# Optimization experiments

Measured on AMD Instinct MI355X. Metric: run time of the kernel, lower is better.

Reference implementation:

```python
import jax, jax.numpy as jnp
import numpy as np

B, S, D, H = 16, 512, 512, 8
DH = D // H
EPS = 1e-5
NEG = -1.0e9


def _layernorm(v, g, b):
    mu = jnp.mean(v, axis=-1, keepdims=True)
    var = jnp.mean(jnp.square(v - mu), axis=-1, keepdims=True)
    return (v - mu) * jax.lax.rsqrt(var + EPS) * g + b


def setup_inputs() -> dict:
    key = jax.random.key(0)
    ks = jax.random.split(key, 12)
    sd = 1.0 / np.sqrt(D)
    return {
        "x": jax.random.normal(ks[0], (B, S, D), dtype=jnp.float32),
        "mask": jax.random.randint(ks[1], (B, S, S), 0, 2, dtype=jnp.int32),
        "ln_g": jnp.ones((D,), jnp.float32),
        "ln_b": jnp.zeros((D,), jnp.float32),
        "lna_g": jnp.ones((S,), jnp.float32),  # LayerNorm over attention scores (last dim = S = model_dim)
        "lna_b": jnp.zeros((S,), jnp.float32),
        "Wq": jax.random.uniform(ks[2], (D, D), jnp.float32, -sd, sd),
        "bq": jnp.zeros((D,), jnp.float32),
        "Wk": jax.random.uniform(ks[3], (D, D), jnp.float32, -sd, sd),
        "bk": jnp.zeros((D,), jnp.float32),
        "Wv": jax.random.uniform(ks[4], (D, D), jnp.float32, -sd, sd),
        "bv": jnp.zeros((D,), jnp.float32),
        "Wd": jax.random.uniform(ks[5], (D, D), jnp.float32, -sd, sd),
        "bd": jnp.zeros((D,), jnp.float32),
    }


def reference(x, mask, ln_g, ln_b, lna_g, lna_b, Wq, bq, Wk, bk, Wv, bv, Wd, bd):
    # pre-LN
    h = _layernorm(x, ln_g, ln_b)  # [B,S,D]
    # projections -> [B,H,S,DH]
    q = (h @ Wq + bq).reshape(B, S, H, DH).transpose(0, 2, 1, 3)
    k = (h @ Wk + bk).reshape(B, S, H, DH).transpose(0, 2, 1, 3)
    v = (h @ Wv + bv).reshape(B, S, H, DH).transpose(0, 2, 1, 3)
    # raw scores [B,H,S,S]
    scores = jnp.einsum("bhqd,bhkd->bhqk", q, k) / jnp.sqrt(jnp.asarray(DH, x.dtype))
    # non-standard: LayerNorm over the key axis of the score matrix
    scores = _layernorm(scores, lna_g, lna_b)
    # mask (broadcast over heads), then softmax
    scores = jnp.where(mask[:, None, :, :] == 0, jnp.asarray(NEG, x.dtype), scores)
    attn = jax.nn.softmax(scores, axis=-1)
    # dropout omitted (eval mode / deterministic reference)
    out = jnp.einsum("bhqk,bhkd->bhqd", attn, v)
    out = out.transpose(0, 2, 1, 3).reshape(B, S, D)
    out = out @ Wd + bd
    return out + x
```

## Files before the change

### kernel.cpp

```cpp
#include <hip/hip_runtime.h>
#include <hip/hip_bf16.h>
#include <stdint.h>


typedef __hip_bfloat16 bf16;
typedef __bf16 bf16x8 __attribute__((ext_vector_type(8)));
typedef float f32x4 __attribute__((ext_vector_type(4)));

#define MFMA16(a, b, c) __builtin_amdgcn_mfma_f32_16x16x32_bf16((a), (b), (c), 0, 0, 0)

static __device__ __forceinline__ bf16 f2b(float v) { return __float2bfloat16(v); }
static __device__ __forceinline__ bf16x8 ld8(const bf16* p) { return *(const bf16x8*)p; }
static __device__ __forceinline__ uint16_t f2bu(float v) {
  return __hip_bfloat16_raw(__float2bfloat16(v)).x;
}
static __device__ __forceinline__ float bu2f(uint32_t u) {
  union { uint32_t i; float f; } c;
  c.i = u << 16;
  return c.f;
}
static __device__ __forceinline__ void stage16(const bf16* g, bf16* l) {
  __builtin_amdgcn_global_load_lds(
      (const __attribute__((address_space(1))) void*)g,
      (__attribute__((address_space(3))) void*)l, 16, 0, 0);
}

__global__ __launch_bounds__(256) void transpose512(
    const float* __restrict__ W0, const float* __restrict__ W1,
    const float* __restrict__ W2, const float* __restrict__ W3,
    bf16* __restrict__ T0, bf16* __restrict__ T1,
    bf16* __restrict__ T2, bf16* __restrict__ T3) {
  __shared__ float t[32][33];
  const float* src; bf16* dst;
  switch (blockIdx.z) {
    case 0: src = W0; dst = T0; break;
    case 1: src = W1; dst = T1; break;
    case 2: src = W2; dst = T2; break;
    default: src = W3; dst = T3; break;
  }
  int tx = threadIdx.x, ty = threadIdx.y;
  int n0 = blockIdx.x * 32, k0 = blockIdx.y * 32;
#pragma unroll
  for (int i = 0; i < 4; i++) {
    int kk = ty * 4 + i;
    t[kk][tx] = src[(k0 + kk) * 512 + n0 + tx];
  }
  __syncthreads();
#pragma unroll
  for (int i = 0; i < 4; i++) {
    int nn = ty * 4 + i;
    dst[(n0 + nn) * 512 + k0 + tx] = f2b(t[tx][nn]);
  }
}

__global__ __launch_bounds__(256) void mask_bits(const int* __restrict__ mask,
                                                 uint32_t* __restrict__ tbits) {
  int t = blockIdx.x * 256 + threadIdx.x;
  int row = t >> 4, l = t & 15;
  const int* mrow = mask + (size_t)row * 512 + l;
  uint32_t o = 0;
#pragma unroll
  for (int j = 0; j < 32; j++) o |= (mrow[j * 16] != 0 ? 1u : 0u) << j;
  tbits[t] = o;
}

__global__ __launch_bounds__(256) void ln_rows(
    const float* __restrict__ x, const float* __restrict__ g,
    const float* __restrict__ be, bf16* __restrict__ h) {
  int row = blockIdx.x;
  int tid = threadIdx.x;
  const float* xr = x + (size_t)row * 512;
  float v0 = xr[tid], v1 = xr[tid + 256];
  float s = v0 + v1, s2 = v0 * v0 + v1 * v1;
#pragma unroll
  for (int m = 1; m < 64; m <<= 1) {
    s += __shfl_xor(s, m);
    s2 += __shfl_xor(s2, m);
  }
  __shared__ float rs[4], rs2[4];
  int w = tid >> 6;
  if ((tid & 63) == 0) { rs[w] = s; rs2[w] = s2; }
  __syncthreads();
  s = rs[0] + rs[1] + rs[2] + rs[3];
  s2 = rs2[0] + rs2[1] + rs2[2] + rs2[3];
  float mean = s * (1.0f / 512.0f);
  float var = s2 * (1.0f / 512.0f) - mean * mean;
  float rstd = rsqrtf(var + 1e-5f);
  bf16* hr = h + (size_t)row * 512;
  hr[tid] = f2b((v0 - mean) * rstd * g[tid] + be[tid]);
  hr[tid + 256] = f2b((v1 - mean) * rstd * g[tid + 256] + be[tid + 256]);
}

__global__ __launch_bounds__(256) void gemm_qkv(
    const bf16* __restrict__ hm,
    const bf16* __restrict__ WT0, const bf16* __restrict__ WT1, const bf16* __restrict__ WT2,
    const float* __restrict__ bq, const float* __restrict__ bk, const float* __restrict__ bv,
    bf16* __restrict__ outq, bf16* __restrict__ outk, bf16* __restrict__ outvT) {
  const int sel = blockIdx.z;
  const bf16* WT = sel == 0 ? WT0 : (sel == 1 ? WT1 : WT2);
  const float* bias = sel == 0 ? bq : (sel == 1 ? bk : bv);
  __shared__ __align__(16) uint16_t SM[128 * 136];
  bf16* As = (bf16*)SM;
  bf16* Bs = (bf16*)(SM + 4096);
  int tid = threadIdx.x;
  int w = tid >> 6, lane = tid & 63, q4 = lane >> 4, l16 = lane & 15;
  int wr = w >> 1, wc = w & 1;
  int m0 = blockIdx.x * 128, n0 = blockIdx.y * 128;
  f32x4 acc[4][4];
#pragma unroll
  for (int i = 0; i < 4; i++)
#pragma unroll
    for (int j = 0; j < 4; j++) acc[i][j] = (f32x4){0.f, 0.f, 0.f, 0.f};

  for (int kc = 0; kc < 16; kc++) {
    int k0 = kc * 32;
#pragma unroll
    for (int u0 = 0; u0 < 2; u0++) {
      int e = u0 * 256 + tid;
      int row = e >> 2, c8 = (e & 3) * 8;
      stage16(&hm[(size_t)(m0 + row) * 512 + k0 + c8], &As[e * 8]);
      stage16(&WT[(size_t)(n0 + row) * 512 + k0 + c8], &Bs[e * 8]);
    }
    __syncthreads();
    bf16x8 af[4], bfr[4];
#pragma unroll
    for (int rt = 0; rt < 4; rt++)
      af[rt] = ld8(&As[(wr * 64 + rt * 16 + l16) * 32 + q4 * 8]);
#pragma unroll
    for (int nt = 0; nt < 4; nt++)
      bfr[nt] = ld8(&Bs[(wc * 64 + nt * 16 + l16) * 32 + q4 * 8]);
#pragma unroll
    for (int rt = 0; rt < 4; rt++)
#pragma unroll
      for (int nt = 0; nt < 4; nt++) acc[rt][nt] = MFMA16(af[rt], bfr[nt], acc[rt][nt]);
    __syncthreads();
  }

  if (sel != 2) {
    const float scale = sel == 0 ? 0.125f : 1.0f;
#pragma unroll
    for (int rt = 0; rt < 4; rt++)
#pragma unroll
      for (int nt = 0; nt < 4; nt++) {
        int ncol = wc * 64 + nt * 16 + l16;
        float bsv = bias[n0 + ncol];
#pragma unroll
        for (int r = 0; r < 4; r++) {
          int mrow = wr * 64 + rt * 16 + q4 * 4 + r;
          SM[mrow * 136 + ncol] = f2bu((acc[rt][nt][r] + bsv) * scale);
        }
      }
    __syncthreads();
    bf16* dst = sel == 0 ? outq : outk;
#pragma unroll
    for (int p = 0; p < 8; p++) {
      int e = p * 256 + tid;
      int row = e >> 4, c8 = (e & 15) * 8;
      bf16x8 vv = *(bf16x8*)&SM[row * 136 + c8];
      int gm = m0 + row, b_ = gm >> 9, s_ = gm & 511;
      int n = n0 + c8, hh = n >> 6, dh = n & 63;
      *(bf16x8*)(dst + ((size_t)((b_ * 8 + hh) * 512 + s_)) * 64 + dh) = vv;
    }
  } else {
#pragma unroll
    for (int rt = 0; rt < 4; rt++)
#pragma unroll
      for (int nt = 0; nt < 4; nt++) {
        int ncol = wc * 64 + nt * 16 + l16;
        float bsv = bias[n0 + ncol];
        union { uint16_t q[4]; uint2 u; } pk;
#pragma unroll
        for (int r = 0; r < 4; r++) pk.q[r] = f2bu(acc[rt][nt][r] + bsv);
        *(uint2*)&SM[ncol * 136 + wr * 64 + rt * 16 + q4 * 4] = pk.u;
      }
    __syncthreads();
#pragma unroll
    for (int p = 0; p < 8; p++) {
      int e = p * 256 + tid;
      int nn = e >> 4, s8 = (e & 15) * 8;
      bf16x8 vv = *(bf16x8*)&SM[nn * 136 + s8];
      int n = n0 + nn, hh = n >> 6, dh = n & 63;
      int gm = m0 + s8, b_ = gm >> 9, s_ = gm & 511;
      *(bf16x8*)(outvT + ((size_t)((b_ * 8 + hh) * 64 + dh)) * 512 + s_) = vv;
    }
  }
}

__global__ __launch_bounds__(256, 2) void attn_fused(
    const bf16* __restrict__ q, const bf16* __restrict__ k, const bf16* __restrict__ vT,
    const uint32_t* __restrict__ tbits, const float* __restrict__ lg,
    const float* __restrict__ lb, bf16* __restrict__ ctx) {
  const int id = blockIdx.x;
  const int xcd = id & 7;
  const int j = id >> 3;
  const int mt = j & 7;
  const int bh = ((j >> 3) << 3) | xcd;
  const int m0 = mt * 64;
  const int b = bh >> 3, hh = bh & 7;
  const int tid = threadIdx.x;
  const int w = tid >> 6, lane = tid & 63, q4 = lane >> 4, l16 = lane & 15;

  __shared__ uint16_t ST[512][66];
  __shared__ __align__(16) bf16 SB[2][2560];

  const bf16* qb = q + ((size_t)bh * 512 + m0 + w * 16) * 64;
  const bf16* kb = k + (size_t)bh * 512 * 64;
  const bf16* vb = vT + (size_t)bh * 64 * 512;

  bf16x8 aq0 = ld8(qb + (size_t)l16 * 64 + q4 * 8);
  bf16x8 aq1 = ld8(qb + (size_t)l16 * 64 + 32 + q4 * 8);

  uint32_t tb[4];
#pragma unroll
  for (int r = 0; r < 4; r++)
    tb[r] = tbits[((size_t)b * 512 + m0 + w * 16 + q4 * 4 + r) * 16 + l16];

  const int col = w * 16 + q4 * 4;

  {
    int key0 = tid >> 3, dh8 = (tid & 7) * 8;
    *(bf16x8*)&SB[0][key0 * 72 + dh8] = ld8(kb + (size_t)key0 * 64 + dh8);
  }
  __syncthreads();

  float s[4] = {0.f, 0.f, 0.f, 0.f}, s2[4] = {0.f, 0.f, 0.f, 0.f};
  for (int c = 0; c < 16; c++) {
    const int buf = c & 1;
    if (c < 15) {
      int key0 = tid >> 3, dh8 = (tid & 7) * 8;
      *(bf16x8*)&SB[buf ^ 1][key0 * 72 + dh8] =
          ld8(kb + (size_t)((c + 1) * 32 + key0) * 64 + dh8);
    }
#pragma unroll
    for (int kg = 0; kg < 2; kg++) {
      const bf16* kp = &SB[buf][(kg * 16 + l16) * 72];
      bf16x8 b0 = ld8(kp + q4 * 8);
      bf16x8 b1 = ld8(kp + 32 + q4 * 8);
      f32x4 acc = (f32x4){0.f, 0.f, 0.f, 0.f};
      acc = MFMA16(aq0, b0, acc);
      acc = MFMA16(aq1, b1, acc);
#pragma unroll
      for (int r = 0; r < 4; r++) {
        float v = acc[r];
        s[r] += v;
        s2[r] += v * v;
      }
      int key = c * 32 + kg * 16 + l16;
      *(uint32_t*)&ST[key][col] = (uint32_t)f2bu(acc[0]) | ((uint32_t)f2bu(acc[1]) << 16);
      *(uint32_t*)&ST[key][col + 2] = (uint32_t)f2bu(acc[2]) | ((uint32_t)f2bu(acc[3]) << 16);
    }
    __syncthreads();
  }

  float mean[4], rstd[4];
#pragma unroll
  for (int r = 0; r < 4; r++) {
    float a = s[r], a2 = s2[r];
#pragma unroll
    for (int mm = 1; mm < 16; mm <<= 1) {
      a += __shfl_xor(a, mm);
      a2 += __shfl_xor(a2, mm);
    }
    float mu = a * (1.0f / 512.0f);
    float var = a2 * (1.0f / 512.0f) - mu * mu;
    mean[r] = mu;
    rstd[r] = rsqrtf(var + 1e-5f);
  }

  float se[4] = {0.f, 0.f, 0.f, 0.f};
#pragma unroll
  for (int i = 0; i < 32; i++) {
    int key = i * 16 + l16;
    float g = lg[key], be = lb[key];
    uint32_t d0 = *(uint32_t*)&ST[key][col];
    uint32_t d1 = *(uint32_t*)&ST[key][col + 2];
    float v[4] = {bu2f(d0 & 0xffff), bu2f(d0 >> 16), bu2f(d1 & 0xffff), bu2f(d1 >> 16)};
    uint16_t p[4];
#pragma unroll
    for (int r = 0; r < 4; r++) {
      float t = (v[r] - mean[r]) * rstd[r] * g + be;
      t = ((tb[r] >> i) & 1u) ? t : -1.0e9f;
      float pf = __expf(t);
      se[r] += pf;
      p[r] = f2bu(pf);
    }
    *(uint32_t*)&ST[key][col] = (uint32_t)p[0] | ((uint32_t)p[1] << 16);
    *(uint32_t*)&ST[key][col + 2] = (uint32_t)p[2] | ((uint32_t)p[3] << 16);
  }
  float inv[4];
#pragma unroll
  for (int r = 0; r < 4; r++) {
    float a = se[r];
#pragma unroll
    for (int mm = 1; mm < 16; mm <<= 1) a += __shfl_xor(a, mm);
    inv[r] = 1.0f / a;
  }

  {
    int dh = tid >> 2, kk8 = (tid & 3) * 8;
    *(bf16x8*)&SB[0][dh * 40 + kk8] = ld8(vb + (size_t)dh * 512 + kk8);
  }
  __syncthreads();

  f32x4 o[4];
#pragma unroll
  for (int nt = 0; nt < 4; nt++) o[nt] = (f32x4){0.f, 0.f, 0.f, 0.f};

  for (int c = 0; c < 16; c++) {
    const int buf = c & 1;
    if (c < 15) {
      int dh = tid >> 2, kk8 = (tid & 3) * 8;
      *(bf16x8*)&SB[buf ^ 1][dh * 40 + kk8] =
          ld8(vb + (size_t)dh * 512 + (c + 1) * 32 + kk8);
    }
    union { uint16_t u[8]; bf16x8 v; } af;
#pragma unroll
    for (int jj = 0; jj < 8; jj++) af.u[jj] = ST[c * 32 + q4 * 8 + jj][w * 16 + l16];
#pragma unroll
    for (int nt = 0; nt < 4; nt++) {
      bf16x8 bv8 = ld8(&SB[buf][(nt * 16 + l16) * 40 + q4 * 8]);
      o[nt] = MFMA16(af.v, bv8, o[nt]);
    }
    __syncthreads();
  }

  bf16* cb = ctx + ((size_t)b * 512 + m0 + w * 16) * 512 + hh * 64;
#pragma unroll
  for (int nt = 0; nt < 4; nt++)
#pragma unroll
    for (int r = 0; r < 4; r++)
      cb[(size_t)(q4 * 4 + r) * 512 + nt * 16 + l16] = f2b(o[nt][r] * inv[r]);
}

__global__ __launch_bounds__(256) void gemm_out(
    const bf16* __restrict__ ctx, const bf16* __restrict__ WT,
    const float* __restrict__ bd, const float* __restrict__ x, float* __restrict__ out) {
  __shared__ __align__(16) bf16 As[128 * 32];
  __shared__ __align__(16) bf16 Bs[128 * 32];
  int tid = threadIdx.x;
  int w = tid >> 6, lane = tid & 63, q4 = lane >> 4, l16 = lane & 15;
  int wr = w >> 1, wc = w & 1;
  int m0 = blockIdx.x * 128, n0 = blockIdx.y * 128;
  f32x4 acc[4][4];
#pragma unroll
  for (int i = 0; i < 4; i++)
#pragma unroll
    for (int j = 0; j < 4; j++) acc[i][j] = (f32x4){0.f, 0.f, 0.f, 0.f};

  for (int kc = 0; kc < 16; kc++) {
    int k0 = kc * 32;
#pragma unroll
    for (int u0 = 0; u0 < 2; u0++) {
      int e = u0 * 256 + tid;
      int row = e >> 2, c8 = (e & 3) * 8;
      stage16(&ctx[(size_t)(m0 + row) * 512 + k0 + c8], &As[e * 8]);
      stage16(&WT[(size_t)(n0 + row) * 512 + k0 + c8], &Bs[e * 8]);
    }
    __syncthreads();
    bf16x8 af[4], bfr[4];
#pragma unroll
    for (int rt = 0; rt < 4; rt++)
      af[rt] = ld8(&As[(wr * 64 + rt * 16 + l16) * 32 + q4 * 8]);
#pragma unroll
    for (int nt = 0; nt < 4; nt++)
      bfr[nt] = ld8(&Bs[(wc * 64 + nt * 16 + l16) * 32 + q4 * 8]);
#pragma unroll
    for (int rt = 0; rt < 4; rt++)
#pragma unroll
      for (int nt = 0; nt < 4; nt++) acc[rt][nt] = MFMA16(af[rt], bfr[nt], acc[rt][nt]);
    __syncthreads();
  }
#pragma unroll
  for (int rt = 0; rt < 4; rt++) {
    int mbase = m0 + wr * 64 + rt * 16 + q4 * 4;
#pragma unroll
    for (int nt = 0; nt < 4; nt++) {
      int n = n0 + wc * 64 + nt * 16 + l16;
      float bsv = bd[n];
#pragma unroll
      for (int r = 0; r < 4; r++) {
        size_t idx = (size_t)(mbase + r) * 512 + n;
        out[idx] = acc[rt][nt][r] + bsv + x[idx];
      }
    }
  }
}

extern "C" void kernel_launch(void* const* d_in, const int* in_sizes, int n_in,
                              void* d_out, int out_size, void* d_ws, size_t ws_size,
                              hipStream_t stream) {
  const float* x = (const float*)d_in[0];
  const int* mask = (const int*)d_in[1];
  const float* ln_g = (const float*)d_in[2];
  const float* ln_b = (const float*)d_in[3];
  const float* lna_g = (const float*)d_in[4];
  const float* lna_b = (const float*)d_in[5];
  const float* Wq = (const float*)d_in[6];
  const float* bq = (const float*)d_in[7];
  const float* Wk = (const float*)d_in[8];
  const float* bk = (const float*)d_in[9];
  const float* Wv = (const float*)d_in[10];
  const float* bv = (const float*)d_in[11];
  const float* Wd = (const float*)d_in[12];
  const float* bd = (const float*)d_in[13];

  char* ws = (char*)d_ws;
  const size_t MB = 1024 * 1024;
  if (ws_size < 44 * MB) return;
  bf16* h = (bf16*)(ws);
  bf16* qd = (bf16*)(ws + 8 * MB);
  bf16* kd = (bf16*)(ws + 16 * MB);
  bf16* vTd = (bf16*)(ws + 24 * MB);
  bf16* ctx = (bf16*)(ws + 32 * MB);
  bf16* WqT = (bf16*)(ws + 40 * MB);
  bf16* WkT = (bf16*)(ws + 40 * MB + 512 * 1024);
  bf16* WvT = (bf16*)(ws + 40 * MB + 1024 * 1024);
  bf16* WdT = (bf16*)(ws + 40 * MB + 1536 * 1024);
  uint32_t* tbits = (uint32_t*)(ws + 42 * MB);

  transpose512<<<dim3(16, 16, 4), dim3(32, 8), 0, stream>>>(Wq, Wk, Wv, Wd, WqT, WkT, WvT, WdT);
  mask_bits<<<512, 256, 0, stream>>>(mask, tbits);
  ln_rows<<<8192, 256, 0, stream>>>(x, ln_g, ln_b, h);
  gemm_qkv<<<dim3(64, 4, 3), 256, 0, stream>>>(h, WqT, WkT, WvT, bq, bk, bv, qd, kd, vTd);
  attn_fused<<<1024, 256, 0, stream>>>(qd, kd, vTd, tbits, lna_g, lna_b, ctx);
  gemm_out<<<dim3(64, 4), 256, 0, stream>>>(ctx, WdT, bd, x, (float*)d_out);
}
```

Before: 189.8 us.

## Fuse score normalisation and exp into PV loop, repack mask with ballot

```diff
diff --git a/kernel.cpp b/kernel.cpp
--- a/kernel.cpp
+++ b/kernel.cpp
@@ -8,6 +8,7 @@
 typedef float f32x4 __attribute__((ext_vector_type(4)));
 
 #define MFMA16(a, b, c) __builtin_amdgcn_mfma_f32_16x16x32_bf16((a), (b), (c), 0, 0, 0)
+#define WAVE_LDS_FENCE() asm volatile("" ::: "memory")
 
 static __device__ __forceinline__ bf16 f2b(float v) { return __float2bfloat16(v); }
 static __device__ __forceinline__ bf16x8 ld8(const bf16* p) { return *(const bf16x8*)p; }
@@ -53,15 +54,14 @@
   }
 }
 
-__global__ __launch_bounds__(256) void mask_bits(const int* __restrict__ mask,
-                                                 uint32_t* __restrict__ tbits) {
-  int t = blockIdx.x * 256 + threadIdx.x;
-  int row = t >> 4, l = t & 15;
-  const int* mrow = mask + (size_t)row * 512 + l;
-  uint32_t o = 0;
-#pragma unroll
-  for (int j = 0; j < 32; j++) o |= (mrow[j * 16] != 0 ? 1u : 0u) << j;
-  tbits[t] = o;
+__global__ __launch_bounds__(256) void mask_pack(const int* __restrict__ mask,
+                                                 uint32_t* __restrict__ bits) {
+  size_t t = (size_t)blockIdx.x * 256 + threadIdx.x;
+  int mv = mask[t];
+  unsigned long long bal = __ballot(mv != 0);
+  if ((threadIdx.x & 63) == 0) {
+    ((unsigned long long*)bits)[t >> 6] = bal;
+  }
 }
 
 __global__ __launch_bounds__(256) void ln_rows(
@@ -188,7 +188,7 @@
 
 __global__ __launch_bounds__(256, 2) void attn_fused(
     const bf16* __restrict__ q, const bf16* __restrict__ k, const bf16* __restrict__ vT,
-    const uint32_t* __restrict__ tbits, const float* __restrict__ lg,
+    const uint32_t* __restrict__ bits, const float* __restrict__ lg,
     const float* __restrict__ lb, bf16* __restrict__ ctx) {
   const int id = blockIdx.x;
   const int xcd = id & 7;
@@ -202,6 +202,11 @@
 
   __shared__ uint16_t ST[512][66];
   __shared__ __align__(16) bf16 SB[2][2560];
+  __shared__ uint32_t GB[512];
+  __shared__ float SMR[4][16][2];
+
+  GB[tid] = (uint32_t)f2bu(lg[tid]) | ((uint32_t)f2bu(lb[tid]) << 16);
+  GB[tid + 256] = (uint32_t)f2bu(lg[tid + 256]) | ((uint32_t)f2bu(lb[tid + 256]) << 16);
 
   const bf16* qb = q + ((size_t)bh * 512 + m0 + w * 16) * 64;
   const bf16* kb = k + (size_t)bh * 512 * 64;
@@ -210,12 +215,11 @@
   bf16x8 aq0 = ld8(qb + (size_t)l16 * 64 + q4 * 8);
   bf16x8 aq1 = ld8(qb + (size_t)l16 * 64 + 32 + q4 * 8);
 
-  uint32_t tb[4];
-#pragma unroll
-  for (int r = 0; r < 4; r++)
-    tb[r] = tbits[((size_t)b * 512 + m0 + w * 16 + q4 * 4 + r) * 16 + l16];
-
-  const int col = w * 16 + q4 * 4;
+  const int myrow = m0 + w * 16 + l16;
+  uint32_t rbits[16];
+#pragma unroll
+  for (int c = 0; c < 16; c++)
+    rbits[c] = bits[((size_t)b * 512 + myrow) * 16 + c];
 
   {
     int key0 = tid >> 3, dh8 = (tid & 7) * 8;
@@ -224,6 +228,7 @@
   __syncthreads();
 
   float s[4] = {0.f, 0.f, 0.f, 0.f}, s2[4] = {0.f, 0.f, 0.f, 0.f};
+  const int col = w * 16 + q4 * 4;
   for (int c = 0; c < 16; c++) {
     const int buf = c & 1;
     if (c < 15) {
@@ -266,35 +271,16 @@
     mean[r] = mu;
     rstd[r] = rsqrtf(var + 1e-5f);
   }
-
-  float se[4] = {0.f, 0.f, 0.f, 0.f};
-#pragma unroll
-  for (int i = 0; i < 32; i++) {
-    int key = i * 16 + l16;
-    float g = lg[key], be = lb[key];
-    uint32_t d0 = *(uint32_t*)&ST[key][col];
-    uint32_t d1 = *(uint32_t*)&ST[key][col + 2];
-    float v[4] = {bu2f(d0 & 0xffff), bu2f(d0 >> 16), bu2f(d1 & 0xffff), bu2f(d1 >> 16)};
-    uint16_t p[4];
+  if (l16 == 0) {
 #pragma unroll
     for (int r = 0; r < 4; r++) {
-      float t = (v[r] - mean[r]) * rstd[r] * g + be;
-      t = ((tb[r] >> i) & 1u) ? t : -1.0e9f;
-      float pf = __expf(t);
-      se[r] += pf;
-      p[r] = f2bu(pf);
-    }
-    *(uint32_t*)&ST[key][col] = (uint32_t)p[0] | ((uint32_t)p[1] << 16);
-    *(uint32_t*)&ST[key][col + 2] = (uint32_t)p[2] | ((uint32_t)p[3] << 16);
-  }
-  float inv[4];
-#pragma unroll
-  for (int r = 0; r < 4; r++) {
-    float a = se[r];
-#pragma unroll
-    for (int mm = 1; mm < 16; mm <<= 1) a += __shfl_xor(a, mm);
-    inv[r] = 1.0f / a;
-  }
+      SMR[w][q4 * 4 + r][0] = mean[r];
+      SMR[w][q4 * 4 + r][1] = rstd[r];
+    }
+  }
+  WAVE_LDS_FENCE();
+  const float mrow = SMR[w][l16][0];
+  const float rrow = SMR[w][l16][1];
 
   {
     int dh = tid >> 2, kk8 = (tid & 3) * 8;
@@ -305,7 +291,9 @@
   f32x4 o[4];
 #pragma unroll
   for (int nt = 0; nt < 4; nt++) o[nt] = (f32x4){0.f, 0.f, 0.f, 0.f};
-
+  float se = 0.f;
+
+#pragma unroll
   for (int c = 0; c < 16; c++) {
     const int buf = c & 1;
     if (c < 15) {
@@ -313,9 +301,19 @@
       *(bf16x8*)&SB[buf ^ 1][dh * 40 + kk8] =
           ld8(vb + (size_t)dh * 512 + (c + 1) * 32 + kk8);
     }
+    const uint32_t mb = rbits[c];
     union { uint16_t u[8]; bf16x8 v; } af;
 #pragma unroll
-    for (int jj = 0; jj < 8; jj++) af.u[jj] = ST[c * 32 + q4 * 8 + jj][w * 16 + l16];
+    for (int jj = 0; jj < 8; jj++) {
+      int key = c * 32 + q4 * 8 + jj;
+      float sv = bu2f(ST[key][w * 16 + l16]);
+      uint32_t gb = GB[key];
+      float t = (sv - mrow) * rrow * bu2f(gb & 0xffffu) + bu2f(gb >> 16);
+      t = ((mb >> (q4 * 8 + jj)) & 1u) ? t : -1.0e9f;
+      float p = __expf(t);
+      se += p;
+      af.u[jj] = f2bu(p);
+    }
 #pragma unroll
     for (int nt = 0; nt < 4; nt++) {
       bf16x8 bv8 = ld8(&SB[buf][(nt * 16 + l16) * 40 + q4 * 8]);
@@ -323,6 +321,13 @@
     }
     __syncthreads();
   }
+
+  se += __shfl_xor(se, 16);
+  se += __shfl_xor(se, 32);
+  float invr = 1.0f / se;
+  float inv[4];
+#pragma unroll
+  for (int r = 0; r < 4; r++) inv[r] = __shfl(invr, q4 * 4 + r);
 
   bf16* cb = ctx + ((size_t)b * 512 + m0 + w * 16) * 512 + hh * 64;
 #pragma unroll
@@ -416,12 +421,12 @@
   bf16* WkT = (bf16*)(ws + 40 * MB + 512 * 1024);
   bf16* WvT = (bf16*)(ws + 40 * MB + 1024 * 1024);
   bf16* WdT = (bf16*)(ws + 40 * MB + 1536 * 1024);
-  uint32_t* tbits = (uint32_t*)(ws + 42 * MB);
+  uint32_t* bits = (uint32_t*)(ws + 42 * MB);
 
   transpose512<<<dim3(16, 16, 4), dim3(32, 8), 0, stream>>>(Wq, Wk, Wv, Wd, WqT, WkT, WvT, WdT);
-  mask_bits<<<512, 256, 0, stream>>>(mask, tbits);
+  mask_pack<<<16384, 256, 0, stream>>>(mask, bits);
   ln_rows<<<8192, 256, 0, stream>>>(x, ln_g, ln_b, h);
   gemm_qkv<<<dim3(64, 4, 3), 256, 0, stream>>>(h, WqT, WkT, WvT, bq, bk, bv, qd, kd, vTd);
-  attn_fused<<<1024, 256, 0, stream>>>(qd, kd, vTd, tbits, lna_g, lna_b, ctx);
+  attn_fused<<<1024, 256, 0, stream>>>(qd, kd, vTd, bits, lna_g, lna_b, ctx);
   gemm_out<<<dim3(64, 4), 256, 0, stream>>>(ctx, WdT, bd, x, (float*)d_out);
 }
```

Result: no change. 186.2 us (-1.9%).
